# Kernel tuning notes

Measured on AMD Instinct MI355X. Metric: run time of the kernel, lower is better.

The kernel has to match this reference:

```python
import jax, jax.numpy as jnp
import numpy as np

B, S, D, H = 4, 2048, 1024, 16  # batch, seq, d_hidden, n_heads


def setup_inputs() -> dict:
    key = jax.random.key(0)
    ks = jax.random.split(key, 7)
    scale = 1.0 / np.sqrt(D)
    return {
        "x": jax.random.normal(ks[0], (B, S, D), dtype=jnp.float32),
        "Wq": jax.random.normal(ks[1], (D, D), dtype=jnp.float32) * scale,
        "bq": jax.random.normal(ks[2], (D,), dtype=jnp.float32) * 0.02,
        "Wk": jax.random.normal(ks[3], (D, D), dtype=jnp.float32) * scale,
        "bk": jax.random.normal(ks[4], (D,), dtype=jnp.float32) * 0.02,
        "Wv": jax.random.normal(ks[5], (D, D), dtype=jnp.float32) * scale,
        "bv": jax.random.normal(ks[6], (D,), dtype=jnp.float32) * 0.02,
    }


def reference(x, Wq, bq, Wk, bk, Wv, bv):
    n_heads = H
    head_dim = D // n_heads

    def proj(inp, W, b):
        # torch nn.Linear: y = x @ W^T + b
        y = jnp.einsum("bsd,ed->bse", inp, W) + b
        # split last dim into (H, Wd) then transpose to (B, H, S, Wd)
        return y.reshape(inp.shape[0], inp.shape[1], n_heads, head_dim).transpose(0, 2, 1, 3)

    q = proj(x, Wq, bq)
    k = proj(x, Wk, bk)
    v = proj(x, Wv, bv)

    # scores: (B, H, S, S)
    scores = jnp.einsum("bhqd,bhkd->bhqk", q, k) / jnp.sqrt(jnp.asarray(head_dim, q.dtype))
    attn = jax.nn.softmax(scores, axis=-1)
    h = jnp.einsum("bhqk,bhkd->bhqd", attn, v)  # (B, H, S, Wd)
    h = h.transpose(0, 2, 1, 3).reshape(x.shape[0], x.shape[1], D)  # merge heads
    return h
```

## Files before the change

### kernel.cpp

```cpp
#include <hip/hip_runtime.h>
#include <hip/hip_bf16.h>

#define B_ 4
#define S_ 2048
#define D_ 1024
#define H_ 16
#define HD 64

typedef __bf16 bf16;
typedef __bf16 bf16x4 __attribute__((ext_vector_type(4)));
typedef __bf16 bf16x8 __attribute__((ext_vector_type(8)));
typedef float f32x4 __attribute__((ext_vector_type(4)));
typedef float f32x16 __attribute__((ext_vector_type(16)));

#define LOG2E 1.4426950408889634f

__device__ inline void gload_lds16(const bf16* g, bf16* l) {
    __builtin_amdgcn_global_load_lds(
        (const __attribute__((address_space(1))) void*)g,
        (__attribute__((address_space(3))) void*)l, 16, 0, 0);
}

__device__ inline int swz(int row, int colb) {
    return row * 64 + ((colb ^ ((row & 7) << 4)) >> 1);
}

__device__ inline unsigned cvt_pk_bf16(float lo, float hi) {
    unsigned r;
    asm("v_cvt_pk_bf16_f32 %0, %1, %2" : "=v"(r) : "v"(lo), "v"(hi));
    return r;
}

__global__ void cast_pack_kernel(const float* __restrict__ x,
                                 const float* __restrict__ Wq,
                                 const float* __restrict__ Wk,
                                 const float* __restrict__ Wv,
                                 bf16* __restrict__ Xb, bf16* __restrict__ Wb) {
    const long XN = (long)B_ * S_ * D_;
    const long WN = (long)D_ * D_;
    long i4 = ((long)blockIdx.x * blockDim.x + threadIdx.x) * 4;
    if (i4 < XN) {
        float4 v = *(const float4*)(x + i4);
        bf16* o = Xb + i4;
        o[0] = (bf16)v.x; o[1] = (bf16)v.y; o[2] = (bf16)v.z; o[3] = (bf16)v.w;
    } else {
        long j = i4 - XN;
        if (j < 3 * WN) {
            int which = (int)(j / WN);
            long jj = j - (long)which * WN;
            const float* src = which == 0 ? Wq : which == 1 ? Wk : Wv;
            float4 v = *(const float4*)(src + jj);
            bf16* o = Wb + j;
            o[0] = (bf16)v.x; o[1] = (bf16)v.y; o[2] = (bf16)v.z; o[3] = (bf16)v.w;
        }
    }
}

#define TM 128
#define TN 256
#define TK 64
#define NKT (D_ / TK)

__global__ __launch_bounds__(512, 2) void gemm_qkv_kernel(
    const bf16* __restrict__ Xb, const bf16* __restrict__ Wb,
    const float* __restrict__ bq, const float* __restrict__ bk,
    const float* __restrict__ bv,
    bf16* __restrict__ Qg, bf16* __restrict__ Kg, bf16* __restrict__ Vt) {
    __shared__ bf16 SMEM[73728];
    bf16* As = SMEM;
    bf16* Bs = SMEM + 3 * 8192;
    const int tid = threadIdx.x;
    const int lane = tid & 63;
    const int wid = tid >> 6;
    const int col = lane & 15, grp = lane >> 4;
    const int wr = wid >> 2, wc = wid & 3;

    const int id = blockIdx.x;
    const int id2 = (id & 7) * 96 + (id >> 3);
    const int m0 = (id2 / 12) * TM;
    const int n0 = (id2 % 12) * TN;

    const int r8 = tid >> 3;
    const int cbs = ((tid & 7) * 16) ^ ((r8 & 7) << 4);
    const bf16* asrc = Xb + (size_t)(m0 + r8) * D_ + (cbs >> 1);
    const bf16* bsrc = Wb + (size_t)(n0 + r8) * D_ + (cbs >> 1);

#define STAGE_ALL(c, kt)                                                                    \
    do {                                                                                    \
        gload_lds16(asrc + (kt) * TK,                       As + (c) * 8192 + wid * 512);   \
        gload_lds16(asrc + (size_t)64 * D_ + (kt) * TK,     As + (c) * 8192 + 4096 + wid * 512); \
        gload_lds16(bsrc + (kt) * TK,                       Bs + (c) * 16384 + wid * 512);  \
        gload_lds16(bsrc + (size_t)64 * D_ + (kt) * TK,     Bs + (c) * 16384 + 4096 + wid * 512); \
        gload_lds16(bsrc + (size_t)128 * D_ + (kt) * TK,    Bs + (c) * 16384 + 8192 + wid * 512); \
        gload_lds16(bsrc + (size_t)192 * D_ + (kt) * TK,    Bs + (c) * 16384 + 12288 + wid * 512); \
    } while (0)

    const f32x4 zf = {0.f, 0.f, 0.f, 0.f};
    f32x4 acc[4][4];
#pragma unroll
    for (int m = 0; m < 4; m++)
#pragma unroll
        for (int n = 0; n < 4; n++) acc[m][n] = zf;

    STAGE_ALL(0, 0);
    STAGE_ALL(1, 1);
    asm volatile("s_waitcnt vmcnt(6)" ::: "memory");
    __builtin_amdgcn_s_barrier();

#pragma unroll
    for (int kt = 0; kt < NKT; ++kt) {
        const int c = kt % 3;
        const bf16* Ac = As + c * 8192;
        const bf16* Bc = Bs + c * 16384;

        bf16x8 a0[4], b0[4], a1[4], b1[4];
#pragma unroll
        for (int m = 0; m < 4; m++) {
            a0[m] = *(const bf16x8*)(Ac + swz(wr * 64 + m * 16 + col, grp * 16));
            a1[m] = *(const bf16x8*)(Ac + swz(wr * 64 + m * 16 + col, 64 + grp * 16));
        }
#pragma unroll
        for (int n = 0; n < 4; n++) {
            b0[n] = *(const bf16x8*)(Bc + swz(wc * 64 + n * 16 + col, grp * 16));
            b1[n] = *(const bf16x8*)(Bc + swz(wc * 64 + n * 16 + col, 64 + grp * 16));
        }

        if (kt < NKT - 2) STAGE_ALL((kt + 2) % 3, kt + 2);

        __builtin_amdgcn_s_setprio(1);
#pragma unroll
        for (int m = 0; m < 4; m++)
#pragma unroll
            for (int n = 0; n < 4; n++)
                acc[m][n] = __builtin_amdgcn_mfma_f32_16x16x32_bf16(a0[m], b0[n], acc[m][n], 0, 0, 0);
#pragma unroll
        for (int m = 0; m < 4; m++)
#pragma unroll
            for (int n = 0; n < 4; n++)
                acc[m][n] = __builtin_amdgcn_mfma_f32_16x16x32_bf16(a1[m], b1[n], acc[m][n], 0, 0, 0);
        __builtin_amdgcn_s_setprio(0);

        if (kt < NKT - 2)
            asm volatile("s_waitcnt vmcnt(6)" ::: "memory");
        else if (kt == NKT - 2)
            asm volatile("s_waitcnt vmcnt(0)" ::: "memory");
        __builtin_amdgcn_s_barrier();
    }
#undef STAGE_ALL

    const int which = n0 >> 10;
    if (which == 2) {
        __syncthreads();
        bf16* Vl = SMEM;
#pragma unroll
        for (int n = 0; n < 4; n++) {
            int dl = wc * 64 + n * 16 + col;
            float bias = bv[(n0 - 2048) + dl];
#pragma unroll
            for (int m = 0; m < 4; m++) {
                bf16x4 pv;
#pragma unroll
                for (int i = 0; i < 4; i++) pv[i] = (bf16)(acc[m][n][i] + bias);
                int sl = wr * 64 + m * 16 + grp * 4;
                *(bf16x4*)(&Vl[dl * 128 + (sl ^ ((dl & 7) << 3))]) = pv;
            }
        }
        __syncthreads();
#pragma unroll
        for (int c0 = 0; c0 < 8; c0++) {
            int cc = c0 * 512 + tid;
            int dl = cc >> 4, s8 = (cc & 15) * 8;
            bf16x8 val = *(const bf16x8*)(&Vl[dl * 128 + (s8 ^ ((dl & 7) << 3))]);
            int s = m0 + s8;
            int b = s >> 11, sl = s & 2047;
            int dglob = (n0 - 2048) + dl;
            int h = dglob >> 6, dd = dglob & 63;
            *(bf16x8*)(&Vt[((size_t)(b * H_ + h) * HD + dd) * S_ + sl]) = val;
        }
    } else {
        const float* bp = which == 0 ? bq : bk;
        bf16* dst = which == 0 ? Qg : Kg;
        const float qsc = which == 0 ? (0.125f * LOG2E) : 1.0f;
#pragma unroll
        for (int n = 0; n < 4; n++) {
            int e = n0 + wc * 64 + n * 16 + col;
            int ee = e & 1023;
            float bias = bp[ee];
            int h = ee >> 6, d = ee & 63;
#pragma unroll
            for (int m = 0; m < 4; m++) {
#pragma unroll
                for (int i = 0; i < 4; i++) {
                    int s = m0 + wr * 64 + m * 16 + grp * 4 + i;
                    int b = s >> 11, sl = s & 2047;
                    dst[((size_t)(b * H_ + h) * S_ + sl) * HD + d] =
                        (bf16)((acc[m][n][i] + bias) * qsc);
                }
            }
        }
    }
}

#define KB 64

__global__ __launch_bounds__(256, 4) void attn_kernel(
    const bf16* __restrict__ Qg, const bf16* __restrict__ Kg,
    const bf16* __restrict__ Vt, float* __restrict__ out) {
    __shared__ bf16 Ks[2][64 * 64];
    __shared__ bf16 Vs[2][64 * 64];
    const int tid = threadIdx.x, lane = tid & 63, wid = tid >> 6;
    const int l31 = lane & 31, hi = lane >> 5;

    const int id = blockIdx.x;
    const int swzid = (id & 7) * 128 + (id >> 3);
    const int bh = swzid >> 4;
    const int q0 = (swzid & 15) * 128 + wid * 32;

    const bf16* Kbase = Kg + (size_t)bh * S_ * HD;
    const bf16* Vbase = Vt + (size_t)bh * HD * S_;

    const int r0 = tid >> 3;
    const int cb = ((tid & 7) * 16) ^ ((r0 & 7) << 4);
    const bf16* ksrc = Kbase + (size_t)r0 * HD + (cb >> 1);
    const bf16* vsrc = Vbase + (size_t)r0 * S_ + (cb >> 1);

#define STAGE(bsel, kv0)                                                       \
    do {                                                                       \
        gload_lds16(ksrc + (size_t)(kv0)*HD,        &Ks[bsel][wid * 512]);     \
        gload_lds16(ksrc + (size_t)((kv0) + 32)*HD, &Ks[bsel][2048 + wid * 512]); \
        gload_lds16(vsrc + (kv0),                   &Vs[bsel][wid * 512]);     \
        gload_lds16(vsrc + 32 * S_ + (kv0),         &Vs[bsel][2048 + wid * 512]); \
    } while (0)

    bf16x8 qa[4];
#pragma unroll
    for (int ks = 0; ks < 4; ks++)
        qa[ks] = *(const bf16x8*)(Qg + ((size_t)bh * S_ + q0 + l31) * HD + ks * 16 + hi * 8);

    const f32x16 z16 = {0.f, 0.f, 0.f, 0.f, 0.f, 0.f, 0.f, 0.f,
                        0.f, 0.f, 0.f, 0.f, 0.f, 0.f, 0.f, 0.f};
    f32x16 o[2];
    o[0] = z16; o[1] = z16;
    f32x4 ls = {0.f, 0.f, 0.f, 0.f};

    int cur = 0;
    STAGE(0, 0);
    __syncthreads();

#pragma unroll 1
    for (int t = 0; t < S_ / KB; ++t) {
        if (t < S_ / KB - 1) STAGE(cur ^ 1, (t + 1) * KB);

        f32x16 sc[2];
        __builtin_amdgcn_s_setprio(1);
#pragma unroll
        for (int kvt = 0; kvt < 2; kvt++) {
#pragma unroll
            for (int ks = 0; ks < 4; ks++) {
                bf16x8 kb = *(const bf16x8*)(&Ks[cur][swz(kvt * 32 + l31, ks * 32 + hi * 16)]);
                if (ks == 0)
                    sc[kvt] = __builtin_amdgcn_mfma_f32_32x32x16_bf16(kb, qa[0], z16, 0, 0, 0);
                else
                    sc[kvt] = __builtin_amdgcn_mfma_f32_32x32x16_bf16(kb, qa[ks], sc[kvt], 0, 0, 0);
            }
        }
        __builtin_amdgcn_s_setprio(0);

#pragma unroll
        for (int kvt = 0; kvt < 2; kvt++) {
            float p[16];
#pragma unroll
            for (int r = 0; r < 16; r++) p[r] = __builtin_amdgcn_exp2f(sc[kvt][r]);
            f32x4 s0 = {p[0], p[1], p[2], p[3]};
            f32x4 s1 = {p[4], p[5], p[6], p[7]};
            f32x4 s2 = {p[8], p[9], p[10], p[11]};
            f32x4 s3 = {p[12], p[13], p[14], p[15]};
            ls += (s0 + s1) + (s2 + s3);
            bf16x8 pa[2];
#pragma unroll
            for (int b = 0; b < 2; b++) {
                unsigned A  = cvt_pk_bf16(p[8 * b + 0], p[8 * b + 1]);
                unsigned Bw = cvt_pk_bf16(p[8 * b + 4], p[8 * b + 5]);
                unsigned C  = cvt_pk_bf16(p[8 * b + 2], p[8 * b + 3]);
                unsigned Dw = cvt_pk_bf16(p[8 * b + 6], p[8 * b + 7]);
                asm("v_permlane32_swap_b32 %0, %1" : "+v"(A), "+v"(Bw));
                asm("v_permlane32_swap_b32 %0, %1" : "+v"(C), "+v"(Dw));
                union { unsigned u[4]; bf16x8 v; } pk;
                pk.u[0] = A; pk.u[1] = C; pk.u[2] = Bw; pk.u[3] = Dw;
                pa[b] = pk.v;
            }
            __builtin_amdgcn_s_setprio(1);
#pragma unroll
            for (int b = 0; b < 2; b++) {
                int kk = kvt * 2 + b;
                bf16x8 vb0 = *(const bf16x8*)(&Vs[cur][swz(l31,      kk * 32 + hi * 16)]);
                bf16x8 vb1 = *(const bf16x8*)(&Vs[cur][swz(32 + l31, kk * 32 + hi * 16)]);
                o[0] = __builtin_amdgcn_mfma_f32_32x32x16_bf16(vb0, pa[b], o[0], 0, 0, 0);
                o[1] = __builtin_amdgcn_mfma_f32_32x32x16_bf16(vb1, pa[b], o[1], 0, 0, 0);
            }
            __builtin_amdgcn_s_setprio(0);
        }

        __syncthreads();
        cur ^= 1;
    }

    float denom = ls[0] + ls[1] + ls[2] + ls[3];
    denom += __shfl_xor(denom, 32);
    float inv = 1.f / denom;

    int b = bh >> 4, h = bh & 15;
    int q = q0 + l31;
    float* obase = out + ((size_t)(b * S_ + q)) * D_ + h * HD;
#pragma unroll
    for (int dt = 0; dt < 2; dt++)
#pragma unroll
        for (int g = 0; g < 4; g++) {
            f32x4 r = {o[dt][4 * g + 0] * inv, o[dt][4 * g + 1] * inv,
                       o[dt][4 * g + 2] * inv, o[dt][4 * g + 3] * inv};
            *(f32x4*)(obase + dt * 32 + 8 * g + 4 * hi) = r;
        }
#undef STAGE
}

extern "C" void kernel_launch(void* const* d_in, const int* in_sizes, int n_in,
                              void* d_out, int out_size, void* d_ws, size_t ws_size,
                              hipStream_t stream) {
    const float* x  = (const float*)d_in[0];
    const float* Wq = (const float*)d_in[1];
    const float* bq = (const float*)d_in[2];
    const float* Wk = (const float*)d_in[3];
    const float* bk = (const float*)d_in[4];
    const float* Wv = (const float*)d_in[5];
    const float* bv = (const float*)d_in[6];
    float* out = (float*)d_out;

    bf16* ws = (bf16*)d_ws;
    bf16* Xb = ws;
    bf16* Wb = Xb + (size_t)B_ * S_ * D_;
    bf16* Qg = Wb + (size_t)3 * D_ * D_;
    bf16* Kg = Qg + (size_t)B_ * S_ * D_;
    bf16* Vt = Kg + (size_t)B_ * S_ * D_;

    hipLaunchKernelGGL(cast_pack_kernel,
                       dim3((B_ * S_ * D_ + 3 * D_ * D_) / (4 * 256)), dim3(256), 0, stream,
                       x, Wq, Wk, Wv, Xb, Wb);
    hipLaunchKernelGGL(gemm_qkv_kernel, dim3(64 * 12), dim3(512), 0, stream,
                       Xb, Wb, bq, bk, bv, Qg, Kg, Vt);
    hipLaunchKernelGGL(attn_kernel, dim3(1024), dim3(256), 0, stream,
                       Qg, Kg, Vt, out);
}
```

Baseline: 160.3 us.

## Split QKV GEMM k-iteration into four interleaved load/MFMA phases with barriers

```diff
diff --git a/kernel.cpp b/kernel.cpp
--- a/kernel.cpp
+++ b/kernel.cpp
@@ -85,15 +85,18 @@
     const bf16* asrc = Xb + (size_t)(m0 + r8) * D_ + (cbs >> 1);
     const bf16* bsrc = Wb + (size_t)(n0 + r8) * D_ + (cbs >> 1);
 
-#define STAGE_ALL(c, kt)                                                                    \
+#define ST_A(c, kt)                                                                         \
     do {                                                                                    \
-        gload_lds16(asrc + (kt) * TK,                       As + (c) * 8192 + wid * 512);   \
-        gload_lds16(asrc + (size_t)64 * D_ + (kt) * TK,     As + (c) * 8192 + 4096 + wid * 512); \
-        gload_lds16(bsrc + (kt) * TK,                       Bs + (c) * 16384 + wid * 512);  \
-        gload_lds16(bsrc + (size_t)64 * D_ + (kt) * TK,     Bs + (c) * 16384 + 4096 + wid * 512); \
-        gload_lds16(bsrc + (size_t)128 * D_ + (kt) * TK,    Bs + (c) * 16384 + 8192 + wid * 512); \
-        gload_lds16(bsrc + (size_t)192 * D_ + (kt) * TK,    Bs + (c) * 16384 + 12288 + wid * 512); \
+        gload_lds16(asrc + (kt) * TK,                    As + (c) * 8192 + wid * 512);      \
+        gload_lds16(asrc + (size_t)64 * D_ + (kt) * TK,  As + (c) * 8192 + 4096 + wid * 512); \
     } while (0)
+#define ST_B0(c, kt) gload_lds16(bsrc + (kt) * TK, Bs + (c) * 16384 + wid * 512)
+#define ST_B12(c, kt)                                                                       \
+    do {                                                                                    \
+        gload_lds16(bsrc + (size_t)64 * D_ + (kt) * TK,  Bs + (c) * 16384 + 4096 + wid * 512); \
+        gload_lds16(bsrc + (size_t)128 * D_ + (kt) * TK, Bs + (c) * 16384 + 8192 + wid * 512); \
+    } while (0)
+#define ST_B3(c, kt) gload_lds16(bsrc + (size_t)192 * D_ + (kt) * TK, Bs + (c) * 16384 + 12288 + wid * 512)
 
     const f32x4 zf = {0.f, 0.f, 0.f, 0.f};
     f32x4 acc[4][4];
@@ -102,51 +105,95 @@
 #pragma unroll
         for (int n = 0; n < 4; n++) acc[m][n] = zf;
 
-    STAGE_ALL(0, 0);
-    STAGE_ALL(1, 1);
+    ST_A(0, 0); ST_B0(0, 0); ST_B12(0, 0); ST_B3(0, 0);
+    ST_A(1, 1); ST_B0(1, 1); ST_B12(1, 1); ST_B3(1, 1);
     asm volatile("s_waitcnt vmcnt(6)" ::: "memory");
     __builtin_amdgcn_s_barrier();
 
 #pragma unroll
     for (int kt = 0; kt < NKT; ++kt) {
         const int c = kt % 3;
+        const int cn = (kt + 2) % 3;
         const bf16* Ac = As + c * 8192;
         const bf16* Bc = Bs + c * 16384;
-
-        bf16x8 a0[4], b0[4], a1[4], b1[4];
+        const bool pf = (kt < NKT - 2);
+
+        bf16x8 a[4], b[4];
+#pragma unroll
+        for (int m = 0; m < 4; m++)
+            a[m] = *(const bf16x8*)(Ac + swz(wr * 64 + m * 16 + col, grp * 16));
+#pragma unroll
+        for (int n = 0; n < 2; n++)
+            b[n] = *(const bf16x8*)(Bc + swz(wc * 64 + n * 16 + col, grp * 16));
+        if (pf) ST_A(cn, kt + 2);
+        __builtin_amdgcn_s_barrier();
+        asm volatile("s_waitcnt lgkmcnt(0)");
+        __builtin_amdgcn_sched_barrier(0);
+        __builtin_amdgcn_s_setprio(1);
 #pragma unroll
         for (int m = 0; m < 4; m++) {
-            a0[m] = *(const bf16x8*)(Ac + swz(wr * 64 + m * 16 + col, grp * 16));
-            a1[m] = *(const bf16x8*)(Ac + swz(wr * 64 + m * 16 + col, 64 + grp * 16));
-        }
-#pragma unroll
-        for (int n = 0; n < 4; n++) {
-            b0[n] = *(const bf16x8*)(Bc + swz(wc * 64 + n * 16 + col, grp * 16));
-            b1[n] = *(const bf16x8*)(Bc + swz(wc * 64 + n * 16 + col, 64 + grp * 16));
-        }
-
-        if (kt < NKT - 2) STAGE_ALL((kt + 2) % 3, kt + 2);
-
-        __builtin_amdgcn_s_setprio(1);
+            acc[m][0] = __builtin_amdgcn_mfma_f32_16x16x32_bf16(a[m], b[0], acc[m][0], 0, 0, 0);
+            acc[m][1] = __builtin_amdgcn_mfma_f32_16x16x32_bf16(a[m], b[1], acc[m][1], 0, 0, 0);
+        }
+        __builtin_amdgcn_s_setprio(0);
+        __builtin_amdgcn_s_barrier();
+#pragma unroll
+        for (int n = 2; n < 4; n++)
+            b[n] = *(const bf16x8*)(Bc + swz(wc * 64 + n * 16 + col, grp * 16));
+        if (pf) ST_B0(cn, kt + 2);
+        __builtin_amdgcn_s_barrier();
+        asm volatile("s_waitcnt lgkmcnt(0)");
+        __builtin_amdgcn_sched_barrier(0);
+        __builtin_amdgcn_s_setprio(1);
+#pragma unroll
+        for (int m = 0; m < 4; m++) {
+            acc[m][2] = __builtin_amdgcn_mfma_f32_16x16x32_bf16(a[m], b[2], acc[m][2], 0, 0, 0);
+            acc[m][3] = __builtin_amdgcn_mfma_f32_16x16x32_bf16(a[m], b[3], acc[m][3], 0, 0, 0);
+        }
+        __builtin_amdgcn_s_setprio(0);
+        __builtin_amdgcn_s_barrier();
 #pragma unroll
         for (int m = 0; m < 4; m++)
-#pragma unroll
-            for (int n = 0; n < 4; n++)
-                acc[m][n] = __builtin_amdgcn_mfma_f32_16x16x32_bf16(a0[m], b0[n], acc[m][n], 0, 0, 0);
-#pragma unroll
-        for (int m = 0; m < 4; m++)
-#pragma unroll
-            for (int n = 0; n < 4; n++)
-                acc[m][n] = __builtin_amdgcn_mfma_f32_16x16x32_bf16(a1[m], b1[n], acc[m][n], 0, 0, 0);
-        __builtin_amdgcn_s_setprio(0);
-
+            a[m] = *(const bf16x8*)(Ac + swz(wr * 64 + m * 16 + col, 64 + grp * 16));
+#pragma unroll
+        for (int n = 0; n < 2; n++)
+            b[n] = *(const bf16x8*)(Bc + swz(wc * 64 + n * 16 + col, 64 + grp * 16));
+        if (pf) ST_B12(cn, kt + 2);
+        __builtin_amdgcn_s_barrier();
+        asm volatile("s_waitcnt lgkmcnt(0)");
+        __builtin_amdgcn_sched_barrier(0);
+        __builtin_amdgcn_s_setprio(1);
+#pragma unroll
+        for (int m = 0; m < 4; m++) {
+            acc[m][0] = __builtin_amdgcn_mfma_f32_16x16x32_bf16(a[m], b[0], acc[m][0], 0, 0, 0);
+            acc[m][1] = __builtin_amdgcn_mfma_f32_16x16x32_bf16(a[m], b[1], acc[m][1], 0, 0, 0);
+        }
+        __builtin_amdgcn_s_setprio(0);
+        __builtin_amdgcn_s_barrier();
+#pragma unroll
+        for (int n = 2; n < 4; n++)
+            b[n] = *(const bf16x8*)(Bc + swz(wc * 64 + n * 16 + col, 64 + grp * 16));
+        if (pf) ST_B3(cn, kt + 2);
+        __builtin_amdgcn_s_barrier();
+        asm volatile("s_waitcnt lgkmcnt(0)");
+        __builtin_amdgcn_sched_barrier(0);
+        __builtin_amdgcn_s_setprio(1);
+#pragma unroll
+        for (int m = 0; m < 4; m++) {
+            acc[m][2] = __builtin_amdgcn_mfma_f32_16x16x32_bf16(a[m], b[2], acc[m][2], 0, 0, 0);
+            acc[m][3] = __builtin_amdgcn_mfma_f32_16x16x32_bf16(a[m], b[3], acc[m][3], 0, 0, 0);
+        }
+        __builtin_amdgcn_s_setprio(0);
         if (kt < NKT - 2)
             asm volatile("s_waitcnt vmcnt(6)" ::: "memory");
         else if (kt == NKT - 2)
             asm volatile("s_waitcnt vmcnt(0)" ::: "memory");
         __builtin_amdgcn_s_barrier();
     }
-#undef STAGE_ALL
+#undef ST_A
+#undef ST_B0
+#undef ST_B12
+#undef ST_B3
 
     const int which = n0 >> 10;
     if (which == 2) {
```

After: 160.5 us. Within noise of the previous version (+0.1%).
